# Optimization experiments

Hardware: AMD Instinct MI355X
Metric: run time of the kernel (lower is better)

Reference implementation:

```python
import jax, jax.numpy as jnp
import numpy as np

N, E, F_IN, HID, H, NCLS, L = 100000, 1600000, 128, 128, 4, 40, 2
C = HID // H  # per-head channels = 32
LN_EPS = 1e-5
SOFTMAX_EPS = 1e-16  # PyG softmax denominator epsilon


def setup_inputs() -> dict:
    key = jax.random.key(0)
    ks = jax.random.split(key, 8)
    s = 1.0 / np.sqrt(F_IN).astype(np.float32)
    return {
        "x": jax.random.normal(ks[0], (N, F_IN), jnp.float32),
        "edge_index": jax.random.randint(ks[1], (2, E), 0, N, jnp.int32),
        "Wq": jax.random.normal(ks[2], (L, F_IN, HID), jnp.float32) * s,
        "bq": jnp.zeros((L, HID), jnp.float32),
        "Wk": jax.random.normal(ks[3], (L, F_IN, HID), jnp.float32) * s,
        "bk": jnp.zeros((L, HID), jnp.float32),
        "Wv": jax.random.normal(ks[4], (L, F_IN, HID), jnp.float32) * s,
        "bv": jnp.zeros((L, HID), jnp.float32),
        "Ws": jax.random.normal(ks[5], (L, F_IN, HID), jnp.float32) * s,
        "bs": jnp.zeros((L, HID), jnp.float32),
        "gamma": jnp.ones((L, HID), jnp.float32),
        "beta": jnp.zeros((L, HID), jnp.float32),
        "Wout": jax.random.normal(ks[6], (HID, NCLS), jnp.float32) * (1.0 / np.sqrt(HID).astype(np.float32)),
        "bout": jnp.zeros((NCLS,), jnp.float32),
    }


def _transformer_conv(x, src, dst, Wq, bq, Wk, bk, Wv, bv, Ws, bs):
    # PyG TransformerConv, concat=False, root_weight=True, beta=False
    n = x.shape[0]
    q = (x @ Wq + bq).reshape(n, H, C)
    k = (x @ Wk + bk).reshape(n, H, C)
    v = (x @ Wv + bv).reshape(n, H, C)
    # per-edge attention logits: [E, H]
    alpha = jnp.einsum('ehc,ehc->eh', q[dst], k[src]) / np.sqrt(C).astype(np.float32)
    # segment softmax over incoming edges of each destination node
    amax = jax.ops.segment_max(alpha, dst, num_segments=n)        # [N, H]
    ex = jnp.exp(alpha - amax[dst])                               # [E, H]
    denom = jax.ops.segment_sum(ex, dst, num_segments=n)         # [N, H]
    w = ex / (denom[dst] + SOFTMAX_EPS)                           # [E, H]
    msg = v[src] * w[:, :, None]                                  # [E, H, C]
    out = jax.ops.segment_sum(msg, dst, num_segments=n)          # [N, H, C]
    out = out.mean(axis=1)                                        # concat=False -> head average, [N, C*?]. Here C*H==HID only via mean over H of C dims -> [N, C]
    # NOTE: concat=False averages heads -> [N, C]; skip proj maps in->C? In PyG, out_channels=hidden here,
    # so lin_* are Linear(in, heads*hidden)... but TransformerConv(in, hidden) means out_channels=hidden/?
    return out


def _conv(x, src, dst, Wq, bq, Wk, bk, Wv, bv, Ws, bs):
    # Faithful version with out_channels = HID per head? No: TransformerConv(in, hidden, heads, concat=False)
    # in PyG uses out_channels=hidden and lin_* : in -> heads*out_channels. To keep HID total width we model
    # per-head dim C = HID // H (standard multi-head factorization with same total width HID).
    n = x.shape[0]
    q = (x @ Wq + bq).reshape(n, H, C)
    k = (x @ Wk + bk).reshape(n, H, C)
    v = (x @ Wv + bv).reshape(n, H, C)
    alpha = jnp.einsum('ehc,ehc->eh', q[dst], k[src]) / np.sqrt(C).astype(np.float32)
    amax = jax.ops.segment_max(alpha, dst, num_segments=n)
    ex = jnp.exp(alpha - amax[dst])
    denom = jax.ops.segment_sum(ex, dst, num_segments=n)
    w = ex / (denom[dst] + SOFTMAX_EPS)
    msg = (v[src] * w[:, :, None]).reshape(-1, H * C)             # [E, HID]
    agg = jax.ops.segment_sum(msg, dst, num_segments=n)          # [N, HID]
    # concat=False -> mean over heads, then broadcast back is not what PyG does; PyG yields [N, out_channels].
    out = agg.reshape(n, H, C).mean(axis=1)                       # [N, C]
    out = jnp.tile(out, (1, H))                                   # widen back to HID? No — instead use skip of width HID.
    return out


def _conv_layer(x, src, dst, Wq, bq, Wk, bk, Wv, bv, Ws, bs):
    """TransformerConv(in, HID, heads=H, concat=False): lin_{q,k,v}: in -> H*HID is too wide for a
    memory target, so we use the equivalent standard factorization HID = H*C (per-head C), giving
    attention output [N, H, C]; concat=False head-mean is applied per head group and the result is
    projected residually via lin_skip (in -> HID)."""
    n = x.shape[0]
    q = (x @ Wq + bq).reshape(n, H, C)
    k = (x @ Wk + bk).reshape(n, H, C)
    v = (x @ Wv + bv).reshape(n, H, C)
    alpha = jnp.einsum('ehc,ehc->eh', q[dst], k[src]) / np.sqrt(C).astype(np.float32)
    amax = jax.ops.segment_max(alpha, dst, num_segments=n)        # [N, H]
    ex = jnp.exp(alpha - amax[dst])                               # [E, H]
    denom = jax.ops.segment_sum(ex, dst, num_segments=n)
    w = ex / (denom[dst] + SOFTMAX_EPS)
    msg = (v[src] * w[:, :, None]).reshape(-1, HID)               # [E, HID] (head-concat)
    agg = jax.ops.segment_sum(msg, dst, num_segments=n)          # [N, HID]
    return agg + x @ Ws + bs                                      # root/skip connection


def _layernorm(h, g, b):
    mu = h.mean(-1, keepdims=True)
    var = ((h - mu) ** 2).mean(-1, keepdims=True)
    return (h - mu) * jax.lax.rsqrt(var + LN_EPS) * g + b


def reference(x, edge_index, Wq, bq, Wk, bk, Wv, bv, Ws, bs, gamma, beta, Wout, bout):
    src, dst = edge_index[0], edge_index[1]
    h = x
    for l in range(L):  # fixed small layer count
        h = _conv_layer(h, src, dst, Wq[l], bq[l], Wk[l], bk[l], Wv[l], bv[l], Ws[l], bs[l])
        h = jax.nn.relu(_layernorm(h, gamma[l], beta[l]))
        # dropout is identity in eval mode
    return h @ Wout + bout  # [N, NCLS]
```

## Files before the change

kernel.cpp:

```cpp
#include <hip/hip_runtime.h>
#include <math.h>

#define N_NODES 100000
#define N_EDGES 1600000
#define NCLS_ 40
#define NSCAN_BLOCKS ((N_NODES + 1023) / 1024)
#define DRANGE 12500

typedef short bf16x8 __attribute__((ext_vector_type(8)));
typedef float f32x4 __attribute__((ext_vector_type(4)));

__device__ __forceinline__ unsigned short f2b(float f) {
    union { float f; unsigned u; } v; v.f = f;
    unsigned r = v.u + 0x7fffu + ((v.u >> 16) & 1u);
    return (unsigned short)(r >> 16);
}
__device__ __forceinline__ float2 up2(unsigned u) {
    union { unsigned u; float f; } a, b;
    a.u = u << 16; b.u = u & 0xffff0000u;
    return make_float2(a.f, b.f);
}
__device__ __forceinline__ unsigned pk2(float x, float y) {
    return (unsigned)f2b(x) | ((unsigned)f2b(y) << 16);
}
__device__ __forceinline__ float b2f(unsigned short s) {
    union { unsigned u; float f; } v; v.u = ((unsigned)s) << 16;
    return v.f;
}


__global__ void zero_i32_kernel(int* __restrict__ p, int n) {
    int i = blockIdx.x * blockDim.x + threadIdx.x;
    if (i < n) p[i] = 0;
}

__global__ __launch_bounds__(256) void wconv_kernel(
    const float* __restrict__ Wq, const float* __restrict__ Wk,
    const float* __restrict__ Wv, const float* __restrict__ Ws,
    unsigned short* __restrict__ Wbf) {
    int tid = blockIdx.x * 256 + threadIdx.x;
    if (tid >= 131072) return;
    int k   = tid & 127;
    int n   = (tid >> 7) & 63;
    int g   = (tid >> 13) & 1;
    int mat = (tid >> 14) & 3;
    int l   = tid >> 16;
    const float* W = (mat == 0) ? Wq : (mat == 1) ? Wk : (mat == 2) ? Wv : Ws;
    Wbf[tid] = f2b(W[l * 16384 + k * 128 + g * 64 + n]);
}

__global__ __launch_bounds__(256) void hist_kernel(
    const int* __restrict__ dst, int* __restrict__ deg) {
    int group = blockIdx.x & 7;
    int gblk  = blockIdx.x >> 3;
    int nblk  = gridDim.x >> 3;
    int lo = group * DRANGE, hi = lo + DRANGE;
    for (int i = gblk * 256 + threadIdx.x; i < N_EDGES; i += nblk * 256) {
        int d = dst[i];
        if (d >= lo && d < hi) atomicAdd(&deg[d], 1);
    }
}

__global__ __launch_bounds__(1024) void scan_block_kernel(
    const int* __restrict__ deg, int* __restrict__ rowptr, int* __restrict__ sums) {
    __shared__ int tmp[1024];
    int t = threadIdx.x;
    int i = blockIdx.x * 1024 + t;
    int v = (i < N_NODES) ? deg[i] : 0;
    tmp[t] = v;
    __syncthreads();
    for (int d = 1; d < 1024; d <<= 1) {
        int add = (t >= d) ? tmp[t - d] : 0;
        __syncthreads();
        tmp[t] += add;
        __syncthreads();
    }
    if (i < N_NODES) rowptr[i] = tmp[t] - v;
    if (t == 1023) sums[blockIdx.x] = tmp[1023];
}

__global__ __launch_bounds__(128) void scan_sums_kernel(int* __restrict__ sums) {
    __shared__ int tmp[128];
    int t = threadIdx.x;
    int v = (t < NSCAN_BLOCKS) ? sums[t] : 0;
    tmp[t] = v;
    __syncthreads();
    for (int d = 1; d < 128; d <<= 1) {
        int add = (t >= d) ? tmp[t - d] : 0;
        __syncthreads();
        tmp[t] += add;
        __syncthreads();
    }
    if (t < NSCAN_BLOCKS) sums[t] = tmp[t] - v;
}

__global__ void scan_add_kernel(int* __restrict__ rowptr, const int* __restrict__ sums,
                                int* __restrict__ cursor) {
    int i = blockIdx.x * blockDim.x + threadIdx.x;
    if (i < N_NODES) {
        int val = rowptr[i] + sums[i >> 10];
        rowptr[i] = val;
        cursor[i] = val;
    }
    if (i == 0) rowptr[N_NODES] = N_EDGES;
}

__global__ __launch_bounds__(256) void scatter_kernel(
    const int* __restrict__ src, const int* __restrict__ dst,
    int* __restrict__ cursor, int* __restrict__ srcs) {
    int group = blockIdx.x & 7;
    int gblk  = blockIdx.x >> 3;
    int nblk  = gridDim.x >> 3;
    int lo = group * DRANGE, hi = lo + DRANGE;
    for (int i = gblk * 256 + threadIdx.x; i < N_EDGES; i += nblk * 256) {
        int d = dst[i];
        if (d >= lo && d < hi) {
            int pos = atomicAdd(&cursor[d], 1);
            srcs[pos] = src[i];
        }
    }
}

__global__ __launch_bounds__(256) void gemm_qkvs_kernel(
    const void* __restrict__ Ap, int a_is_bf16,
    const unsigned short* __restrict__ Wbf,
    const float* __restrict__ b0, const float* __restrict__ b1,
    const float* __restrict__ b2, const float* __restrict__ b3,
    unsigned short* __restrict__ out) {
    __shared__ unsigned short As[64][138];
    __shared__ unsigned short Bs[2][64][138];
    int t = threadIdx.x;
    int row0 = blockIdx.x * 64;

    if (a_is_bf16) {
        const unsigned short* A = (const unsigned short*)Ap;
        for (int i = 0; i < 8; ++i) {
            int idx = t + i * 256;
            int r = idx >> 5, k4 = (idx & 31) << 2;
            ushort4 v = make_ushort4(0, 0, 0, 0);
            if (row0 + r < N_NODES) v = *(const ushort4*)&A[(size_t)(row0 + r) * 128 + k4];
            *(ushort4*)&As[r][k4] = v;
        }
    } else {
        const float* A = (const float*)Ap;
        for (int i = 0; i < 8; ++i) {
            int idx = t + i * 256;
            int r = idx >> 5, k4 = (idx & 31) << 2;
            float4 v = make_float4(0.f, 0.f, 0.f, 0.f);
            if (row0 + r < N_NODES) v = *(const float4*)&A[(size_t)(row0 + r) * 128 + k4];
            ushort4 o;
            o.x = f2b(v.x); o.y = f2b(v.y); o.z = f2b(v.z); o.w = f2b(v.w);
            *(ushort4*)&As[r][k4] = o;
        }
    }

    int wv = t >> 6, lane = t & 63;
    int ln = lane & 15, quad = lane >> 4;

    ushort4 pf[8];
    {
        const unsigned short* Wg = Wbf;
        for (int i = 0; i < 8; ++i) {
            int idx = t + i * 256;
            pf[i] = *(const ushort4*)&Wg[((idx >> 5) << 7) + ((idx & 31) << 2)];
        }
        for (int i = 0; i < 8; ++i) {
            int idx = t + i * 256;
            *(ushort4*)&Bs[0][idx >> 5][(idx & 31) << 2] = pf[i];
        }
    }
    __syncthreads();

    #pragma unroll
    for (int g = 0; g < 8; ++g) {
        int mat = g >> 1;
        int cur = g & 1;
        const float* bias = (mat == 0) ? b0 : (mat == 1) ? b1 : (mat == 2) ? b2 : b3;
        int cb = (g & 1) * 64;

        if (g < 7) {
            const unsigned short* Wg = Wbf + (size_t)(g + 1) * 8192;
            for (int i = 0; i < 8; ++i) {
                int idx = t + i * 256;
                pf[i] = *(const ushort4*)&Wg[((idx >> 5) << 7) + ((idx & 31) << 2)];
            }
        }

        f32x4 acc[4];
        for (int c = 0; c < 4; ++c) acc[c] = (f32x4){0.f, 0.f, 0.f, 0.f};
        for (int ks = 0; ks < 4; ++ks) {
            int k0 = ks * 32 + quad * 8;
            bf16x8 a = *(bf16x8*)&As[wv * 16 + ln][k0];
            for (int c = 0; c < 4; ++c) {
                bf16x8 b = *(bf16x8*)&Bs[cur][c * 16 + ln][k0];
                acc[c] = __builtin_amdgcn_mfma_f32_16x16x32_bf16(a, b, acc[c], 0, 0, 0);
            }
        }

        for (int c = 0; c < 4; ++c) {
            int colInMat = cb + c * 16 + ln;
            float bb = bias[colInMat];
            int pos;
            if (mat == 0)      pos = colInMat;
            else if (mat == 3) pos = 384 + colInMat;
            else               pos = 128 + ((colInMat >> 1) << 2) + ((mat == 2) ? 2 : 0) + (colInMat & 1);
            for (int r = 0; r < 4; ++r) {
                int row = row0 + wv * 16 + quad * 4 + r;
                if (row < N_NODES)
                    out[(size_t)row * 512 + pos] = f2b(acc[c][r] + bb);
            }
        }

        if (g < 7) {
            int nxt = cur ^ 1;
            for (int i = 0; i < 8; ++i) {
                int idx = t + i * 256;
                *(ushort4*)&Bs[nxt][idx >> 5][(idx & 31) << 2] = pf[i];
            }
        }
        __syncthreads();
    }
}

__global__ __launch_bounds__(256) void edge_fused_kernel(
    const unsigned short* __restrict__ qkvs,
    const int* __restrict__ srcs, const int* __restrict__ rowptr,
    const float* __restrict__ gamma, const float* __restrict__ beta,
    unsigned short* __restrict__ hout) {
    int n = (blockIdx.x * 256 + threadIdx.x) >> 6;
    int lane = threadIdx.x & 63;
    if (n >= N_NODES) return;
    float2 q2 = up2(*(const unsigned*)&qkvs[(size_t)n * 512 + 2 * lane]);
    float2 sk = up2(*(const unsigned*)&qkvs[(size_t)n * 512 + 384 + 2 * lane]);
    int e0 = rowptr[n], e1 = rowptr[n + 1];
    float accx = 0.f, accy = 0.f, dsum = 0.f;
    const float sc = 0.17677669529663687f;
    int idx = e0;
    for (; idx + 3 < e1; idx += 4) {
        int s0 = srcs[idx], s1 = srcs[idx + 1], s2 = srcs[idx + 2], s3 = srcs[idx + 3];
        uint2 kv0 = *(const uint2*)&qkvs[(size_t)s0 * 512 + 128 + 4 * lane];
        uint2 kv1 = *(const uint2*)&qkvs[(size_t)s1 * 512 + 128 + 4 * lane];
        uint2 kv2 = *(const uint2*)&qkvs[(size_t)s2 * 512 + 128 + 4 * lane];
        uint2 kv3 = *(const uint2*)&qkvs[(size_t)s3 * 512 + 128 + 4 * lane];
        float2 k0 = up2(kv0.x), k1 = up2(kv1.x), k2 = up2(kv2.x), k3 = up2(kv3.x);
        float p0 = q2.x * k0.x + q2.y * k0.y;
        float p1 = q2.x * k1.x + q2.y * k1.y;
        float p2 = q2.x * k2.x + q2.y * k2.y;
        float p3 = q2.x * k3.x + q2.y * k3.y;
        p0 += __shfl_xor(p0, 1); p1 += __shfl_xor(p1, 1); p2 += __shfl_xor(p2, 1); p3 += __shfl_xor(p3, 1);
        p0 += __shfl_xor(p0, 2); p1 += __shfl_xor(p1, 2); p2 += __shfl_xor(p2, 2); p3 += __shfl_xor(p3, 2);
        p0 += __shfl_xor(p0, 4); p1 += __shfl_xor(p1, 4); p2 += __shfl_xor(p2, 4); p3 += __shfl_xor(p3, 4);
        p0 += __shfl_xor(p0, 8); p1 += __shfl_xor(p1, 8); p2 += __shfl_xor(p2, 8); p3 += __shfl_xor(p3, 8);
        float e0v = expf(p0 * sc), e1v = expf(p1 * sc);
        float e2v = expf(p2 * sc), e3v = expf(p3 * sc);
        float2 v0 = up2(kv0.y), v1 = up2(kv1.y), v2 = up2(kv2.y), v3 = up2(kv3.y);
        accx += e0v * v0.x + e1v * v1.x + e2v * v2.x + e3v * v3.x;
        accy += e0v * v0.y + e1v * v1.y + e2v * v2.y + e3v * v3.y;
        dsum += (e0v + e1v) + (e2v + e3v);
    }
    for (; idx < e1; ++idx) {
        int s0 = srcs[idx];
        uint2 kv0 = *(const uint2*)&qkvs[(size_t)s0 * 512 + 128 + 4 * lane];
        float2 k0 = up2(kv0.x);
        float p0 = q2.x * k0.x + q2.y * k0.y;
        p0 += __shfl_xor(p0, 1);
        p0 += __shfl_xor(p0, 2);
        p0 += __shfl_xor(p0, 4);
        p0 += __shfl_xor(p0, 8);
        float e0v = expf(p0 * sc);
        float2 v0 = up2(kv0.y);
        accx += e0v * v0.x;
        accy += e0v * v0.y;
        dsum += e0v;
    }
    float dinv = 1.0f / (dsum + 1e-16f);
    float vx = accx * dinv + sk.x, vy = accy * dinv + sk.y;
    float sum = vx + vy;
    for (int msk = 1; msk < 64; msk <<= 1) sum += __shfl_xor(sum, msk);
    float mu = sum * (1.0f / 128.0f);
    float dx = vx - mu, dy = vy - mu;
    float sq = dx * dx + dy * dy;
    for (int msk = 1; msk < 64; msk <<= 1) sq += __shfl_xor(sq, msk);
    float rs = rsqrtf(sq * (1.0f / 128.0f) + 1e-5f);
    int c = 2 * lane;
    float o0 = dx * rs * gamma[c]     + beta[c];
    float o1 = dy * rs * gamma[c + 1] + beta[c + 1];
    o0 = fmaxf(o0, 0.f);
    o1 = fmaxf(o1, 0.f);
    *(unsigned*)&hout[(size_t)n * 128 + c] = pk2(o0, o1);
}

__global__ __launch_bounds__(256) void out_gemm_kernel(
    const unsigned short* __restrict__ h, const float* __restrict__ Wout,
    const float* __restrict__ bout, float* __restrict__ out) {
    __shared__ float hs[32][132];
    __shared__ float ws[128 * NCLS_];
    __shared__ float bsd[NCLS_];
    int t = threadIdx.x;
    int n0 = blockIdx.x * 32;
    for (int i = t; i < 128 * NCLS_; i += 256) ws[i] = Wout[i];
    if (t < NCLS_) bsd[t] = bout[t];
    for (int i = t; i < 1024; i += 256) {
        int r = i >> 5, k4 = (i & 31) << 2;
        float4 a = make_float4(0.f, 0.f, 0.f, 0.f);
        if (n0 + r < N_NODES) {
            ushort4 u = *(const ushort4*)&h[(size_t)(n0 + r) * 128 + k4];
            a = make_float4(b2f(u.x), b2f(u.y), b2f(u.z), b2f(u.w));
        }
        *(float4*)&hs[r][k4] = a;
    }
    __syncthreads();
    int r = t >> 3, j0 = (t & 7) * 5;
    float acc[5];
    for (int j = 0; j < 5; ++j) acc[j] = bsd[j0 + j];
    for (int k = 0; k < 128; ++k) {
        float a = hs[r][k];
        for (int j = 0; j < 5; ++j) acc[j] += a * ws[k * NCLS_ + j0 + j];
    }
    int n = n0 + r;
    if (n < N_NODES) {
        for (int j = 0; j < 5; ++j) out[(size_t)n * NCLS_ + j0 + j] = acc[j];
    }
}

extern "C" void kernel_launch(void* const* d_in, const int* in_sizes, int n_in,
                              void* d_out, int out_size, void* d_ws, size_t ws_size,
                              hipStream_t stream) {
    const float* x    = (const float*)d_in[0];
    const int*   ei   = (const int*)d_in[1];
    const int*   src  = ei;
    const int*   dst  = ei + N_EDGES;
    const float* Wq   = (const float*)d_in[2];
    const float* bq   = (const float*)d_in[3];
    const float* Wk   = (const float*)d_in[4];
    const float* bk   = (const float*)d_in[5];
    const float* Wv   = (const float*)d_in[6];
    const float* bv   = (const float*)d_in[7];
    const float* Wsk  = (const float*)d_in[8];
    const float* bsk  = (const float*)d_in[9];
    const float* gmm  = (const float*)d_in[10];
    const float* bta  = (const float*)d_in[11];
    const float* Wout = (const float*)d_in[12];
    const float* bout = (const float*)d_in[13];
    float* outp = (float*)d_out;

    char* p = (char*)d_ws;
    auto carve = [&](size_t bytes) {
        char* r = p;
        p += (bytes + 255) & ~(size_t)255;
        return r;
    };
    unsigned short* qkvs = (unsigned short*)carve((size_t)N_NODES * 512 * 2);
    unsigned short* h    = (unsigned short*)carve((size_t)N_NODES * 128 * 2);
    unsigned short* Wbf  = (unsigned short*)carve((size_t)131072 * 2);
    int* deg     = (int*)carve((size_t)N_NODES * 4);
    int* rowptr  = (int*)carve((size_t)(N_NODES + 1) * 4);
    int* cursor  = (int*)carve((size_t)N_NODES * 4);
    int* srcs    = (int*)carve((size_t)N_EDGES * 4);
    int* sums    = (int*)carve((size_t)NSCAN_BLOCKS * 4);

    wconv_kernel<<<512, 256, 0, stream>>>(Wq, Wk, Wv, Wsk, Wbf);

    zero_i32_kernel<<<(N_NODES + 255) / 256, 256, 0, stream>>>(deg, N_NODES);
    hist_kernel<<<2048, 256, 0, stream>>>(dst, deg);
    scan_block_kernel<<<NSCAN_BLOCKS, 1024, 0, stream>>>(deg, rowptr, sums);
    scan_sums_kernel<<<1, 128, 0, stream>>>(sums);
    scan_add_kernel<<<(N_NODES + 255) / 256, 256, 0, stream>>>(rowptr, sums, cursor);
    scatter_kernel<<<2048, 256, 0, stream>>>(src, dst, cursor, srcs);

    for (int l = 0; l < 2; ++l) {
        const void* hin = l ? (const void*)h : (const void*)x;
        gemm_qkvs_kernel<<<(N_NODES + 63) / 64, 256, 0, stream>>>(
            hin, l, Wbf + (size_t)l * 65536,
            bq + l * 128, bk + l * 128, bv + l * 128, bsk + l * 128, qkvs);
        edge_fused_kernel<<<(N_NODES + 3) / 4, 256, 0, stream>>>(
            qkvs, srcs, rowptr, gmm + l * 128, bta + l * 128, h);
    }
    out_gemm_kernel<<<(N_NODES + 31) / 32, 256, 0, stream>>>(h, Wout, bout, outp);
}
```

Measured before the change: 716.4 us.

## Interleave K/V in 4-wide groups and split wavefront halves across edges

Changes the qkvs layout so each K/V group holds 4 contiguous channels. Each half-wavefront (32 lanes) now processes a different edge with 16-byte loads, so one wave gathers two edges per step and the halves are combined with a cross-half shuffle at the end. This targets gather efficiency and cuts shuffle-reduction steps per edge. It also switches to the fast __expf. The LayerNorm sum now double-counts the replicated halves and divides by 256 to compensate. The tail loop clamps out-of-range indices and masks them with zero weight.

```diff
diff --git a/kernel.cpp b/kernel.cpp
--- a/kernel.cpp
+++ b/kernel.cpp
@@ -203,7 +203,7 @@
             int pos;
             if (mat == 0)      pos = colInMat;
             else if (mat == 3) pos = 384 + colInMat;
-            else               pos = 128 + ((colInMat >> 1) << 2) + ((mat == 2) ? 2 : 0) + (colInMat & 1);
+            else               pos = 128 + ((colInMat >> 2) << 3) + ((mat == 2) ? 4 : 0) + (colInMat & 3);
             for (int r = 0; r < 4; ++r) {
                 int row = row0 + wv * 16 + quad * 4 + r;
                 if (row < N_NODES)
@@ -230,64 +230,78 @@
     int n = (blockIdx.x * 256 + threadIdx.x) >> 6;
     int lane = threadIdx.x & 63;
     if (n >= N_NODES) return;
-    float2 q2 = up2(*(const unsigned*)&qkvs[(size_t)n * 512 + 2 * lane]);
-    float2 sk = up2(*(const unsigned*)&qkvs[(size_t)n * 512 + 384 + 2 * lane]);
+    int half = lane >> 5, hl = lane & 31;
+    const unsigned short* qrow = qkvs + (size_t)n * 512;
+    uint2 qu = *(const uint2*)&qrow[4 * hl];
+    float2 q01 = up2(qu.x), q23 = up2(qu.y);
+    uint2 su = *(const uint2*)&qrow[384 + 4 * hl];
+    float2 sk01 = up2(su.x), sk23 = up2(su.y);
     int e0 = rowptr[n], e1 = rowptr[n + 1];
-    float accx = 0.f, accy = 0.f, dsum = 0.f;
+    float a0 = 0.f, a1 = 0.f, a2 = 0.f, a3 = 0.f, dsum = 0.f;
     const float sc = 0.17677669529663687f;
     int idx = e0;
     for (; idx + 3 < e1; idx += 4) {
-        int s0 = srcs[idx], s1 = srcs[idx + 1], s2 = srcs[idx + 2], s3 = srcs[idx + 3];
-        uint2 kv0 = *(const uint2*)&qkvs[(size_t)s0 * 512 + 128 + 4 * lane];
-        uint2 kv1 = *(const uint2*)&qkvs[(size_t)s1 * 512 + 128 + 4 * lane];
-        uint2 kv2 = *(const uint2*)&qkvs[(size_t)s2 * 512 + 128 + 4 * lane];
-        uint2 kv3 = *(const uint2*)&qkvs[(size_t)s3 * 512 + 128 + 4 * lane];
-        float2 k0 = up2(kv0.x), k1 = up2(kv1.x), k2 = up2(kv2.x), k3 = up2(kv3.x);
-        float p0 = q2.x * k0.x + q2.y * k0.y;
-        float p1 = q2.x * k1.x + q2.y * k1.y;
-        float p2 = q2.x * k2.x + q2.y * k2.y;
-        float p3 = q2.x * k3.x + q2.y * k3.y;
-        p0 += __shfl_xor(p0, 1); p1 += __shfl_xor(p1, 1); p2 += __shfl_xor(p2, 1); p3 += __shfl_xor(p3, 1);
-        p0 += __shfl_xor(p0, 2); p1 += __shfl_xor(p1, 2); p2 += __shfl_xor(p2, 2); p3 += __shfl_xor(p3, 2);
-        p0 += __shfl_xor(p0, 4); p1 += __shfl_xor(p1, 4); p2 += __shfl_xor(p2, 4); p3 += __shfl_xor(p3, 4);
-        p0 += __shfl_xor(p0, 8); p1 += __shfl_xor(p1, 8); p2 += __shfl_xor(p2, 8); p3 += __shfl_xor(p3, 8);
-        float e0v = expf(p0 * sc), e1v = expf(p1 * sc);
-        float e2v = expf(p2 * sc), e3v = expf(p3 * sc);
-        float2 v0 = up2(kv0.y), v1 = up2(kv1.y), v2 = up2(kv2.y), v3 = up2(kv3.y);
-        accx += e0v * v0.x + e1v * v1.x + e2v * v2.x + e3v * v3.x;
-        accy += e0v * v0.y + e1v * v1.y + e2v * v2.y + e3v * v3.y;
-        dsum += (e0v + e1v) + (e2v + e3v);
-    }
-    for (; idx < e1; ++idx) {
-        int s0 = srcs[idx];
-        uint2 kv0 = *(const uint2*)&qkvs[(size_t)s0 * 512 + 128 + 4 * lane];
-        float2 k0 = up2(kv0.x);
-        float p0 = q2.x * k0.x + q2.y * k0.y;
-        p0 += __shfl_xor(p0, 1);
-        p0 += __shfl_xor(p0, 2);
-        p0 += __shfl_xor(p0, 4);
-        p0 += __shfl_xor(p0, 8);
-        float e0v = expf(p0 * sc);
-        float2 v0 = up2(kv0.y);
-        accx += e0v * v0.x;
-        accy += e0v * v0.y;
-        dsum += e0v;
-    }
+        int sA = srcs[idx + half];
+        int sB = srcs[idx + 2 + half];
+        uint4 kvA = *(const uint4*)&qkvs[(size_t)sA * 512 + 128 + 8 * hl];
+        uint4 kvB = *(const uint4*)&qkvs[(size_t)sB * 512 + 128 + 8 * hl];
+        float2 kA01 = up2(kvA.x), kA23 = up2(kvA.y);
+        float2 kB01 = up2(kvB.x), kB23 = up2(kvB.y);
+        float pA = q01.x * kA01.x + q01.y * kA01.y + q23.x * kA23.x + q23.y * kA23.y;
+        float pB = q01.x * kB01.x + q01.y * kB01.y + q23.x * kB23.x + q23.y * kB23.y;
+        pA += __shfl_xor(pA, 1); pB += __shfl_xor(pB, 1);
+        pA += __shfl_xor(pA, 2); pB += __shfl_xor(pB, 2);
+        pA += __shfl_xor(pA, 4); pB += __shfl_xor(pB, 4);
+        float eA = __expf(pA * sc), eB = __expf(pB * sc);
+        float2 vA01 = up2(kvA.z), vA23 = up2(kvA.w);
+        float2 vB01 = up2(kvB.z), vB23 = up2(kvB.w);
+        a0 += eA * vA01.x + eB * vB01.x;
+        a1 += eA * vA01.y + eB * vB01.y;
+        a2 += eA * vA23.x + eB * vB23.x;
+        a3 += eA * vA23.y + eB * vB23.y;
+        dsum += eA + eB;
+    }
+    for (; idx < e1; idx += 2) {
+        int i = idx + half;
+        bool valid = i < e1;
+        int sA = srcs[valid ? i : e1 - 1];
+        uint4 kvA = *(const uint4*)&qkvs[(size_t)sA * 512 + 128 + 8 * hl];
+        float2 kA01 = up2(kvA.x), kA23 = up2(kvA.y);
+        float pA = q01.x * kA01.x + q01.y * kA01.y + q23.x * kA23.x + q23.y * kA23.y;
+        pA += __shfl_xor(pA, 1);
+        pA += __shfl_xor(pA, 2);
+        pA += __shfl_xor(pA, 4);
+        float eA = valid ? __expf(pA * sc) : 0.f;
+        float2 vA01 = up2(kvA.z), vA23 = up2(kvA.w);
+        a0 += eA * vA01.x; a1 += eA * vA01.y;
+        a2 += eA * vA23.x; a3 += eA * vA23.y;
+        dsum += eA;
+    }
+    a0 += __shfl_xor(a0, 32); a1 += __shfl_xor(a1, 32);
+    a2 += __shfl_xor(a2, 32); a3 += __shfl_xor(a3, 32);
+    dsum += __shfl_xor(dsum, 32);
     float dinv = 1.0f / (dsum + 1e-16f);
-    float vx = accx * dinv + sk.x, vy = accy * dinv + sk.y;
-    float sum = vx + vy;
-    for (int msk = 1; msk < 64; msk <<= 1) sum += __shfl_xor(sum, msk);
-    float mu = sum * (1.0f / 128.0f);
-    float dx = vx - mu, dy = vy - mu;
-    float sq = dx * dx + dy * dy;
-    for (int msk = 1; msk < 64; msk <<= 1) sq += __shfl_xor(sq, msk);
-    float rs = rsqrtf(sq * (1.0f / 128.0f) + 1e-5f);
-    int c = 2 * lane;
-    float o0 = dx * rs * gamma[c]     + beta[c];
-    float o1 = dy * rs * gamma[c + 1] + beta[c + 1];
-    o0 = fmaxf(o0, 0.f);
-    o1 = fmaxf(o1, 0.f);
-    *(unsigned*)&hout[(size_t)n * 128 + c] = pk2(o0, o1);
+    float o0 = a0 * dinv + sk01.x, o1 = a1 * dinv + sk01.y;
+    float o2 = a2 * dinv + sk23.x, o3 = a3 * dinv + sk23.y;
+    float sum = o0 + o1 + o2 + o3;
+    for (int m = 1; m < 64; m <<= 1) sum += __shfl_xor(sum, m);
+    float mu = sum * (1.0f / 256.0f);
+    float d0 = o0 - mu, d1 = o1 - mu, d2 = o2 - mu, d3 = o3 - mu;
+    float sq = d0 * d0 + d1 * d1 + d2 * d2 + d3 * d3;
+    for (int m = 1; m < 64; m <<= 1) sq += __shfl_xor(sq, m);
+    float rs = rsqrtf(sq * (1.0f / 256.0f) + 1e-5f);
+    if (half == 0) {
+        float4 g4 = *(const float4*)&gamma[4 * hl];
+        float4 b4 = *(const float4*)&beta[4 * hl];
+        float r0 = fmaxf(d0 * rs * g4.x + b4.x, 0.f);
+        float r1 = fmaxf(d1 * rs * g4.y + b4.y, 0.f);
+        float r2 = fmaxf(d2 * rs * g4.z + b4.z, 0.f);
+        float r3 = fmaxf(d3 * rs * g4.w + b4.w, 0.f);
+        uint2 w;
+        w.x = pk2(r0, r1);
+        w.y = pk2(r2, r3);
+        *(uint2*)&hout[(size_t)n * 128 + 4 * hl] = w;
+    }
 }
 
 __global__ __launch_bounds__(256) void out_gemm_kernel(
```

New measurement: 703.9 us. About the same (-1.7%).
